# Performance work log

Hardware: AMD Instinct MI355X
Metric: run time of the kernel (lower is better)

Reference implementation:

```python
import jax, jax.numpy as jnp
import numpy as np
from jax import lax

N = 2048
BS = 64
NUM_ITR = 25


def setup_inputs() -> dict:
    key = jax.random.key(0)
    k1, k2, k3, k4, k5 = jax.random.split(key, 5)
    scale = 0.5 / np.sqrt(N)  # keep iteration matrices contractive so the recurrence stays bounded
    H = jax.random.normal(k1, (N, N), dtype=jnp.float32) / np.sqrt(N)
    Dinv = jax.random.normal(k2, (N, N), dtype=jnp.float32) * scale
    U = jax.random.normal(k3, (N, N), dtype=jnp.float32) * scale
    invM = jax.random.normal(k4, (N, N), dtype=jnp.float32) * scale
    y = jax.random.normal(k5, (BS, N), dtype=jnp.float32)
    return {"num_itr": NUM_ITR, "bs": BS, "y": y, "H": H, "Dinv": Dinv, "U": U, "invM": invM}


def reference(num_itr, bs, y, H, Dinv, U, invM):
    n = H.shape[0]
    s0 = jnp.zeros((bs, n), dtype=y.dtype)
    yMF = y @ H.T                 # [bs, n]
    s_init = yMF @ Dinv           # initial Gauss-Seidel estimate

    def step(s, _):
        s_next = (yMF - s @ U) @ invM
        return s_next, s_next

    s_final, traj_iters = lax.scan(step, s_init, None, length=num_itr)
    # traj matches the torch list: [zeros, s_1, ..., s_num_itr]
    traj = jnp.concatenate([s0[None], traj_iters], axis=0)  # [num_itr+1, bs, n]
    return s_final, traj
```

## Files before the change

kernel.cpp:

```cpp
#include <hip/hip_runtime.h>
#include <hip/hip_bf16.h>

#define NDIM 2048
#define BS   64
#define NM4  (NDIM * NDIM / 4)
#define BSN  ((size_t)BS * NDIM)
#define SMEM_BYTES 69632

typedef __bf16 bf16_t;
typedef __bf16 bf16x4 __attribute__((ext_vector_type(4)));
typedef __bf16 bf16x8 __attribute__((ext_vector_type(8)));
typedef float  f32x4  __attribute__((ext_vector_type(4)));

__device__ __forceinline__ void gload16(const void* g, void* lds) {
  __builtin_amdgcn_global_load_lds(
      (const __attribute__((address_space(1))) void*)g,
      (__attribute__((address_space(3))) void*)lds, 16, 0, 0);
}

#define WB4 asm volatile("s_waitcnt vmcnt(4)\n\ts_barrier" ::: "memory")
#define WB2 asm volatile("s_waitcnt vmcnt(2)\n\ts_barrier" ::: "memory")
#define WB0 asm volatile("s_waitcnt vmcnt(0)\n\ts_barrier" ::: "memory")

__global__ __launch_bounds__(512) void prep(
    const float* __restrict__ H, const float* __restrict__ U,
    const float* __restrict__ Dinv, const float* __restrict__ invM,
    const float* __restrict__ y,
    bf16_t* __restrict__ H16, bf16_t* __restrict__ U16,
    bf16_t* __restrict__ Dt, bf16_t* __restrict__ iMt,
    bf16_t* __restrict__ y16, float* __restrict__ traj0) {
  __shared__ bf16_t tile[64][72];
  int b = blockIdx.x, tid = threadIdx.x;
  if (b < 1024) {
#pragma unroll
    for (int i = 0; i < 4; ++i) {
      int idx = b * 2048 + i * 512 + tid;
      const float* src = (idx < NM4) ? H : U;
      bf16_t* dst = (idx < NM4) ? H16 : U16;
      int j = (idx < NM4) ? idx : idx - NM4;
      float4 v = ((const float4*)src)[j];
      bf16x4 o = {(bf16_t)v.x, (bf16_t)v.y, (bf16_t)v.z, (bf16_t)v.w};
      ((bf16x4*)dst)[j] = o;
    }
    int yi = b * 512 + tid;
    if (yi < BS * NDIM / 4) {
      float4 w = ((const float4*)y)[yi];
      bf16x4 o2 = {(bf16_t)w.x, (bf16_t)w.y, (bf16_t)w.z, (bf16_t)w.w};
      ((bf16x4*)y16)[yi] = o2;
      ((float4*)traj0)[yi] = make_float4(0.f, 0.f, 0.f, 0.f);
    }
  } else {
    int id = b - 1024;
    const float* src = (id < 1024) ? Dinv : invM;
    bf16_t* dst = (id < 1024) ? Dt : iMt;
    id &= 1023;
    int bx = id & 31, by = id >> 5;
    int r = tid >> 3, c8 = (tid & 7) * 8;
    const float* sp = src + (size_t)(by * 64 + r) * NDIM + bx * 64 + c8;
    float4 v0 = *(const float4*)sp;
    float4 v1 = *(const float4*)(sp + 4);
    bf16_t* t = &tile[r][c8];
    t[0] = (bf16_t)v0.x; t[1] = (bf16_t)v0.y; t[2] = (bf16_t)v0.z; t[3] = (bf16_t)v0.w;
    t[4] = (bf16_t)v1.x; t[5] = (bf16_t)v1.y; t[6] = (bf16_t)v1.z; t[7] = (bf16_t)v1.w;
    __syncthreads();
    bf16x8 o;
#pragma unroll
    for (int j = 0; j < 8; ++j) o[j] = tile[c8 + j][r];
    *(bf16x8*)(dst + (size_t)(bx * 64 + r) * NDIM + by * 64 + c8) = o;
  }
}

__device__ __forceinline__ void wgemm_role(
    const bf16_t* __restrict__ A, const bf16_t* __restrict__ Bt,
    bf16_t* __restrict__ C, int blk, char* smem) {
  int tid = threadIdx.x, lane = tid & 63, wave = tid >> 6;
  int m0 = (blk >> 4) * 128, n0 = (blk & 15) * 128;
  int rl = lane & 15, q = lane >> 4;
  const bf16_t* Ag = A  + (size_t)(m0 + wave * 16 + rl) * NDIM + q * 8;
  const bf16_t* Bg = Bt + (size_t)(n0 + wave * 16 + rl) * NDIM + q * 8;
  char* ldsA = smem + wave * 1024;
  char* ldsB = smem + 8192 + wave * 1024;

  f32x4 acc[2][4];
#pragma unroll
  for (int i = 0; i < 2; ++i)
#pragma unroll
    for (int j = 0; j < 4; ++j) acc[i][j] = (f32x4){0.f, 0.f, 0.f, 0.f};

  int wr2 = (wave & 3) * 2, wc4 = (wave >> 2) * 4;

#define STAGE(s)                                  \
  {                                               \
    int _b = (s) & 3, _k = (s) * 32;              \
    gload16(Ag + _k, ldsA + _b * 16384);          \
    gload16(Bg + _k, ldsB + _b * 16384);          \
  }
#define COMPUTE(bb)                                                            \
  {                                                                            \
    bf16x8* As = (bf16x8*)(smem + (bb) * 16384);                               \
    bf16x8* Bs = (bf16x8*)(smem + (bb) * 16384 + 8192);                        \
    bf16x8 af0 = As[wr2 * 64 + lane];                                          \
    bf16x8 af1 = As[(wr2 + 1) * 64 + lane];                                    \
    bf16x8 bf0 = Bs[wc4 * 64 + lane];                                          \
    bf16x8 bf1 = Bs[(wc4 + 1) * 64 + lane];                                    \
    bf16x8 bf2 = Bs[(wc4 + 2) * 64 + lane];                                    \
    bf16x8 bf3 = Bs[(wc4 + 3) * 64 + lane];                                    \
    acc[0][0] = __builtin_amdgcn_mfma_f32_16x16x32_bf16(af0, bf0, acc[0][0], 0, 0, 0); \
    acc[0][1] = __builtin_amdgcn_mfma_f32_16x16x32_bf16(af0, bf1, acc[0][1], 0, 0, 0); \
    acc[0][2] = __builtin_amdgcn_mfma_f32_16x16x32_bf16(af0, bf2, acc[0][2], 0, 0, 0); \
    acc[0][3] = __builtin_amdgcn_mfma_f32_16x16x32_bf16(af0, bf3, acc[0][3], 0, 0, 0); \
    acc[1][0] = __builtin_amdgcn_mfma_f32_16x16x32_bf16(af1, bf0, acc[1][0], 0, 0, 0); \
    acc[1][1] = __builtin_amdgcn_mfma_f32_16x16x32_bf16(af1, bf1, acc[1][1], 0, 0, 0); \
    acc[1][2] = __builtin_amdgcn_mfma_f32_16x16x32_bf16(af1, bf2, acc[1][2], 0, 0, 0); \
    acc[1][3] = __builtin_amdgcn_mfma_f32_16x16x32_bf16(af1, bf3, acc[1][3], 0, 0, 0); \
  }

  STAGE(0); STAGE(1); STAGE(2);
  int s = 3;
#pragma unroll 1
  for (int k = 0; k < 60; k += 4) {
    WB4; STAGE(s); ++s; COMPUTE(0);
    WB4; STAGE(s); ++s; COMPUTE(1);
    WB4; STAGE(s); ++s; COMPUTE(2);
    WB4; STAGE(s); ++s; COMPUTE(3);
  }
  WB4; STAGE(63); COMPUTE(0);
  WB4; COMPUTE(1);
  WB2; COMPUTE(2);
  WB0; COMPUTE(3);
#undef STAGE
#undef COMPUTE

#pragma unroll
  for (int i = 0; i < 2; ++i)
#pragma unroll
    for (int j = 0; j < 4; ++j)
#pragma unroll
      for (int r = 0; r < 4; ++r)
        C[(size_t)(m0 + (wr2 + i) * 16 + q * 4 + r) * NDIM + n0 + (wc4 + j) * 16 + rl] =
            (bf16_t)acc[i][j][r];
}

__device__ __forceinline__ void skinny_role(
    const bf16_t* __restrict__ A, const bf16_t* __restrict__ Bt, int n0, char* smem,
    const float* __restrict__ add, float sign,
    float* o32, float* o32b, bf16_t* o16) {
  int tid = threadIdx.x, lane = tid & 63, wave = tid >> 6;
  int rl = lane & 15, q = lane >> 4;
#pragma unroll
  for (int i = 0; i < 8; ++i) {
    const bf16_t* g = Bt + (size_t)(n0 + rl) * NDIM + (i * 8 + wave) * 32 + q * 8;
    gload16(g, smem + (size_t)(i * 512 + wave * 64) * 16);
  }
  __syncthreads();

  int ms = (wave & 3) * 16, kh = wave >> 2;
  const bf16x8* Ap = (const bf16x8*)(A + (size_t)(ms + rl) * NDIM) + q + kh * 128;
  const bf16x8* Bp = (const bf16x8*)smem + lane + kh * 2048;

  f32x4 acc[8];
#pragma unroll
  for (int i = 0; i < 8; ++i) acc[i] = (f32x4){0.f, 0.f, 0.f, 0.f};
#pragma unroll
  for (int c = 0; c < 32; ++c)
    acc[c & 7] = __builtin_amdgcn_mfma_f32_16x16x32_bf16(Ap[c * 4], Bp[c * 64], acc[c & 7], 0, 0, 0);
  f32x4 s = ((acc[0] + acc[1]) + (acc[2] + acc[3])) + ((acc[4] + acc[5]) + (acc[6] + acc[7]));

  f32x4* red = (f32x4*)(smem + 65536);
  if (wave >= 4) red[(wave & 3) * 64 + lane] = s;
  __syncthreads();
  if (wave < 4) {
    s += red[wave * 64 + lane];
    int mrow = ms + q * 4, col = n0 + rl;
#pragma unroll
    for (int r = 0; r < 4; ++r) {
      size_t o = (size_t)(mrow + r) * NDIM + col;
      float v = sign * s[r];
      if (add) v += add[o];
      if (o32)  o32[o]  = v;
      if (o32b) o32b[o] = v;
      if (o16)  o16[o]  = (bf16_t)v;
    }
  }
}

__device__ __forceinline__ void transpose_role(const bf16_t* __restrict__ src,
                                               bf16_t* __restrict__ dst, int blk, char* smem) {
  bf16_t (*tile)[72] = (bf16_t(*)[72])smem;
  int tid = threadIdx.x;
  int bx = blk & 31, by = blk >> 5;
  int r = tid >> 3, c8 = (tid & 7) * 8;
  *(bf16x8*)&tile[r][c8] = *(const bf16x8*)(src + (size_t)(by * 64 + r) * NDIM + bx * 64 + c8);
  __syncthreads();
  bf16x8 o;
#pragma unroll
  for (int j = 0; j < 8; ++j) o[j] = tile[c8 + j][r];
  *(bf16x8*)(dst + (size_t)(bx * 64 + r) * NDIM + by * 64 + c8) = o;
}

__global__ __launch_bounds__(512, 4) void megaA(
    const bf16_t* __restrict__ U16, const bf16_t* __restrict__ iMt16,
    const bf16_t* __restrict__ y16, const bf16_t* __restrict__ H16,
    bf16_t* __restrict__ Wrm, bf16_t* __restrict__ yMF16) {
  __shared__ char smem[SMEM_BYTES];
  int b = blockIdx.x;
  if (b < 256) wgemm_role(U16, iMt16, Wrm, b, smem);
  else         skinny_role(y16, H16, (b - 256) * 16, smem, nullptr, 1.f, nullptr, nullptr, yMF16);
}

__global__ __launch_bounds__(512, 4) void megaB(
    const bf16_t* __restrict__ Wrm, const bf16_t* __restrict__ yMF16,
    const bf16_t* __restrict__ iMt16, const bf16_t* __restrict__ Dt16,
    bf16_t* __restrict__ Wt, float* __restrict__ c32, bf16_t* __restrict__ c16,
    bf16_t* __restrict__ z0) {
  __shared__ char smem[SMEM_BYTES];
  int b = blockIdx.x;
  if (b < 1024)      transpose_role(Wrm, Wt, b, smem);
  else if (b < 1152) skinny_role(yMF16, iMt16, (b - 1024) * 16, smem, nullptr, 1.f, c32, nullptr, c16);
  else               skinny_role(yMF16, Dt16, (b - 1152) * 16, smem, nullptr, 1.f, nullptr, nullptr, z0);
}

__global__ __launch_bounds__(512, 4) void megaC(
    const bf16_t* __restrict__ Wt, const bf16_t* __restrict__ Wrm,
    const bf16_t* __restrict__ z0, const bf16_t* __restrict__ c16,
    const float* __restrict__ c32,
    bf16_t* __restrict__ W2t, float* __restrict__ traj1, bf16_t* __restrict__ z0b,
    float* __restrict__ c2_32, bf16_t* __restrict__ c2_16) {
  __shared__ char smem[SMEM_BYTES];
  int b = blockIdx.x;
  if (b < 256)      wgemm_role(Wt, Wrm, W2t, b, smem);
  else if (b < 384) skinny_role(z0, Wt, (b - 256) * 16, smem, c32, -1.f, traj1, nullptr, z0b);
  else              skinny_role(c16, Wt, (b - 384) * 16, smem, c32, -1.f, c2_32, nullptr, c2_16);
}

__global__ __launch_bounds__(512, 4) void megaD(
    const bf16_t* __restrict__ W2t, const bf16_t* __restrict__ z0,
    const bf16_t* __restrict__ c2_16, const float* __restrict__ c2_32,
    bf16_t* __restrict__ W2rm, float* __restrict__ traj2, float* __restrict__ traj3,
    bf16_t* __restrict__ zA, float* __restrict__ c4_32) {
  __shared__ char smem[SMEM_BYTES];
  int b = blockIdx.x;
  if (b < 1024)      transpose_role(W2t, W2rm, b, smem);
  else if (b < 1152) skinny_role(z0, W2t, (b - 1024) * 16, smem, c2_32, 1.f, traj2, nullptr, zA);
  else if (b < 1280) skinny_role(z0 + BSN, W2t, (b - 1152) * 16, smem, c2_32, 1.f, traj3, nullptr, zA + BSN);
  else               skinny_role(c2_16, W2t, (b - 1280) * 16, smem, c2_32, 1.f, c4_32, nullptr, nullptr);
}

__global__ __launch_bounds__(512, 4) void megaE(
    const bf16_t* __restrict__ W2t, const bf16_t* __restrict__ W2rm,
    const bf16_t* __restrict__ zA_in, const float* __restrict__ c2_32,
    bf16_t* __restrict__ W4t, float* __restrict__ traj4, float* __restrict__ traj5,
    bf16_t* __restrict__ zA) {
  __shared__ char smem[SMEM_BYTES];
  int b = blockIdx.x;
  if (b < 256)      wgemm_role(W2t, W2rm, W4t, b, smem);
  else if (b < 384) skinny_role(zA_in, W2t, (b - 256) * 16, smem, c2_32, 1.f, traj4, nullptr, zA + 2 * BSN);
  else              skinny_role(zA_in + BSN, W2t, (b - 384) * 16, smem, c2_32, 1.f, traj5, nullptr, zA + 3 * BSN);
}

__global__ __launch_bounds__(512, 4) void quad_step(
    const bf16_t* __restrict__ zin, const bf16_t* __restrict__ W4t,
    const float* __restrict__ c4_32, float* __restrict__ trajb,
    bf16_t* __restrict__ zout, float* __restrict__ sfin) {
  __shared__ char smem[SMEM_BYTES];
  int b = blockIdx.x, ci = b & 3, p = b >> 2;
  skinny_role(zin + (size_t)ci * BSN, W4t, p * 16, smem, c4_32, 1.f,
              trajb + (size_t)ci * BSN, (ci == 3) ? sfin : nullptr,
              zout + (size_t)ci * BSN);
}

extern "C" void kernel_launch(void* const* d_in, const int* in_sizes, int n_in,
                              void* d_out, int out_size, void* d_ws, size_t ws_size,
                              hipStream_t stream) {
  const float* y    = (const float*)d_in[2];
  const float* H    = (const float*)d_in[3];
  const float* Dinv = (const float*)d_in[4];
  const float* U    = (const float*)d_in[5];
  const float* invM = (const float*)d_in[6];

  float* out     = (float*)d_out;
  float* s_final = out;
  float* traj    = out + BSN;

  char* ws = (char*)d_ws;
  size_t off = 0;
  auto alloc = [&](size_t bytes) -> void* {
    void* p = ws + off;
    off += (bytes + 255) & ~(size_t)255;
    return p;
  };
  bf16_t* U16   = (bf16_t*)alloc((size_t)NDIM * NDIM * 2);
  bf16_t* Dt16  = (bf16_t*)alloc((size_t)NDIM * NDIM * 2);
  bf16_t* iMt16 = (bf16_t*)alloc((size_t)NDIM * NDIM * 2);
  bf16_t* H16   = (bf16_t*)alloc((size_t)NDIM * NDIM * 2);
  bf16_t* Wrm   = (bf16_t*)alloc((size_t)NDIM * NDIM * 2);
  bf16_t* Wt    = (bf16_t*)alloc((size_t)NDIM * NDIM * 2);
  bf16_t* y16   = (bf16_t*)alloc(BSN * 2);
  bf16_t* yMF16 = (bf16_t*)alloc(BSN * 2);
  bf16_t* c16   = (bf16_t*)alloc(BSN * 2);
  bf16_t* c2_16 = (bf16_t*)alloc(BSN * 2);
  float*  c32   = (float*)alloc(BSN * 4);
  float*  c2_32 = (float*)alloc(BSN * 4);
  float*  c4_32 = (float*)alloc(BSN * 4);
  bf16_t* z0    = (bf16_t*)alloc(2 * BSN * 2);
  bf16_t* zA    = (bf16_t*)alloc(4 * BSN * 2);
  bf16_t* zB    = (bf16_t*)alloc(4 * BSN * 2);
  bf16_t* W2t   = H16;
  bf16_t* W2rm  = U16;
  bf16_t* W4t   = Dt16;

  prep<<<3072, 512, 0, stream>>>(H, U, Dinv, invM, y, H16, U16, Dt16, iMt16, y16, traj);
  megaA<<<384, 512, 0, stream>>>(U16, iMt16, y16, H16, Wrm, yMF16);
  megaB<<<1280, 512, 0, stream>>>(Wrm, yMF16, iMt16, Dt16, Wt, c32, c16, z0);
  megaC<<<512, 512, 0, stream>>>(Wt, Wrm, z0, c16, c32, W2t, traj + BSN, z0 + BSN, c2_32, c2_16);
  megaD<<<1408, 512, 0, stream>>>(W2t, z0, c2_16, c2_32, W2rm, traj + 2 * BSN, traj + 3 * BSN,
                                  zA, c4_32);
  megaE<<<512, 512, 0, stream>>>(W2t, W2rm, zA, c2_32, W4t, traj + 4 * BSN, traj + 5 * BSN, zA);

  bf16_t* zcur = zA;
  bf16_t* znxt = zB;
  for (int g = 0; g < 5; ++g) {
    float* sfin = (g == 4) ? s_final : nullptr;
    quad_step<<<512, 512, 0, stream>>>(zcur, W4t, c4_32, traj + (size_t)(6 + 4 * g) * BSN,
                                       znxt, sfin);
    bf16_t* tmp = zcur; zcur = znxt; znxt = tmp;
  }
}
```

Baseline: 389.2 us.

## Fuse transposes into GEMM epilogue and use inline-asm LDS reads

The dense GEMM role now writes a transposed copy of its output tile through an LDS staging buffer, so the separate transpose blocks in megaB and megaD are removed and those launches shrink to only the skinny products. The GEMM inner loop also switches to inline-asm ds_read_b128 with immediate offsets and an explicit lgkmcnt wait. This drops two full-matrix read/write passes but adds an extra epilogue with barriers and a second global store per GEMM block. The explicit waitcnt may also limit how well the compiler overlaps LDS reads with MFMAs.

```diff
diff --git a/kernel.cpp b/kernel.cpp
--- a/kernel.cpp
+++ b/kernel.cpp
@@ -16,6 +16,9 @@
   __builtin_amdgcn_global_load_lds(
       (const __attribute__((address_space(1))) void*)g,
       (__attribute__((address_space(3))) void*)lds, 16, 0, 0);
+}
+__device__ __forceinline__ uint32_t lds_off(void* p) {
+  return (uint32_t)(uintptr_t)(__attribute__((address_space(3))) void*)p;
 }
 
 #define WB4 asm volatile("s_waitcnt vmcnt(4)\n\ts_barrier" ::: "memory")
@@ -72,7 +75,7 @@
 
 __device__ __forceinline__ void wgemm_role(
     const bf16_t* __restrict__ A, const bf16_t* __restrict__ Bt,
-    bf16_t* __restrict__ C, int blk, char* smem) {
+    bf16_t* __restrict__ C, bf16_t* __restrict__ Ct, int blk, char* smem) {
   int tid = threadIdx.x, lane = tid & 63, wave = tid >> 6;
   int m0 = (blk >> 4) * 128, n0 = (blk & 15) * 128;
   int rl = lane & 15, q = lane >> 4;
@@ -81,13 +84,15 @@
   char* ldsA = smem + wave * 1024;
   char* ldsB = smem + 8192 + wave * 1024;
 
+  int wr2 = (wave & 3) * 2, wc4 = (wave >> 2) * 4;
+  uint32_t abase = lds_off(smem) + wr2 * 1024 + lane * 16;
+  uint32_t bbase = lds_off(smem) + 8192 + wc4 * 1024 + lane * 16;
+
   f32x4 acc[2][4];
 #pragma unroll
   for (int i = 0; i < 2; ++i)
 #pragma unroll
     for (int j = 0; j < 4; ++j) acc[i][j] = (f32x4){0.f, 0.f, 0.f, 0.f};
-
-  int wr2 = (wave & 3) * 2, wc4 = (wave >> 2) * 4;
 
 #define STAGE(s)                                  \
   {                                               \
@@ -97,22 +102,26 @@
   }
 #define COMPUTE(bb)                                                            \
   {                                                                            \
-    bf16x8* As = (bf16x8*)(smem + (bb) * 16384);                               \
-    bf16x8* Bs = (bf16x8*)(smem + (bb) * 16384 + 8192);                        \
-    bf16x8 af0 = As[wr2 * 64 + lane];                                          \
-    bf16x8 af1 = As[(wr2 + 1) * 64 + lane];                                    \
-    bf16x8 bf0 = Bs[wc4 * 64 + lane];                                          \
-    bf16x8 bf1 = Bs[(wc4 + 1) * 64 + lane];                                    \
-    bf16x8 bf2 = Bs[(wc4 + 2) * 64 + lane];                                    \
-    bf16x8 bf3 = Bs[(wc4 + 3) * 64 + lane];                                    \
-    acc[0][0] = __builtin_amdgcn_mfma_f32_16x16x32_bf16(af0, bf0, acc[0][0], 0, 0, 0); \
-    acc[0][1] = __builtin_amdgcn_mfma_f32_16x16x32_bf16(af0, bf1, acc[0][1], 0, 0, 0); \
-    acc[0][2] = __builtin_amdgcn_mfma_f32_16x16x32_bf16(af0, bf2, acc[0][2], 0, 0, 0); \
-    acc[0][3] = __builtin_amdgcn_mfma_f32_16x16x32_bf16(af0, bf3, acc[0][3], 0, 0, 0); \
-    acc[1][0] = __builtin_amdgcn_mfma_f32_16x16x32_bf16(af1, bf0, acc[1][0], 0, 0, 0); \
-    acc[1][1] = __builtin_amdgcn_mfma_f32_16x16x32_bf16(af1, bf1, acc[1][1], 0, 0, 0); \
-    acc[1][2] = __builtin_amdgcn_mfma_f32_16x16x32_bf16(af1, bf2, acc[1][2], 0, 0, 0); \
-    acc[1][3] = __builtin_amdgcn_mfma_f32_16x16x32_bf16(af1, bf3, acc[1][3], 0, 0, 0); \
+    uint32_t av = abase + (bb) * 16384;                                        \
+    uint32_t bv = bbase + (bb) * 16384;                                        \
+    bf16x8 af0, af1, bg0, bg1, bg2, bg3;                                       \
+    asm volatile("ds_read_b128 %0, %1"             : "=v"(af0) : "v"(av));     \
+    asm volatile("ds_read_b128 %0, %1 offset:1024" : "=v"(af1) : "v"(av));     \
+    asm volatile("ds_read_b128 %0, %1"             : "=v"(bg0) : "v"(bv));     \
+    asm volatile("ds_read_b128 %0, %1 offset:1024" : "=v"(bg1) : "v"(bv));     \
+    asm volatile("ds_read_b128 %0, %1 offset:2048" : "=v"(bg2) : "v"(bv));     \
+    asm volatile("ds_read_b128 %0, %1 offset:3072" : "=v"(bg3) : "v"(bv));     \
+    asm volatile("s_waitcnt lgkmcnt(0)"                                        \
+                 : "+v"(af0), "+v"(af1), "+v"(bg0), "+v"(bg1), "+v"(bg2),      \
+                   "+v"(bg3));                                                 \
+    acc[0][0] = __builtin_amdgcn_mfma_f32_16x16x32_bf16(af0, bg0, acc[0][0], 0, 0, 0); \
+    acc[0][1] = __builtin_amdgcn_mfma_f32_16x16x32_bf16(af0, bg1, acc[0][1], 0, 0, 0); \
+    acc[0][2] = __builtin_amdgcn_mfma_f32_16x16x32_bf16(af0, bg2, acc[0][2], 0, 0, 0); \
+    acc[0][3] = __builtin_amdgcn_mfma_f32_16x16x32_bf16(af0, bg3, acc[0][3], 0, 0, 0); \
+    acc[1][0] = __builtin_amdgcn_mfma_f32_16x16x32_bf16(af1, bg0, acc[1][0], 0, 0, 0); \
+    acc[1][1] = __builtin_amdgcn_mfma_f32_16x16x32_bf16(af1, bg1, acc[1][1], 0, 0, 0); \
+    acc[1][2] = __builtin_amdgcn_mfma_f32_16x16x32_bf16(af1, bg2, acc[1][2], 0, 0, 0); \
+    acc[1][3] = __builtin_amdgcn_mfma_f32_16x16x32_bf16(af1, bg3, acc[1][3], 0, 0, 0); \
   }
 
   STAGE(0); STAGE(1); STAGE(2);
@@ -139,6 +148,24 @@
       for (int r = 0; r < 4; ++r)
         C[(size_t)(m0 + (wr2 + i) * 16 + q * 4 + r) * NDIM + n0 + (wc4 + j) * 16 + rl] =
             (bf16_t)acc[i][j][r];
+
+  if (Ct) {
+    __syncthreads();
+    bf16_t (*tileT)[136] = (bf16_t(*)[136])smem;
+#pragma unroll
+    for (int i = 0; i < 2; ++i)
+#pragma unroll
+      for (int j = 0; j < 4; ++j)
+#pragma unroll
+        for (int r = 0; r < 4; ++r)
+          tileT[(wc4 + j) * 16 + rl][(wr2 + i) * 16 + q * 4 + r] = (bf16_t)acc[i][j][r];
+    __syncthreads();
+#pragma unroll
+    for (int t = 0; t < 4; ++t) {
+      int v = t * 512 + tid, row = v >> 4, c8 = (v & 15) * 8;
+      *(bf16x8*)(Ct + (size_t)(n0 + row) * NDIM + m0 + c8) = *(bf16x8*)&tileT[row][c8];
+    }
+  }
 }
 
 __device__ __forceinline__ void skinny_role(
@@ -184,51 +211,36 @@
   }
 }
 
-__device__ __forceinline__ void transpose_role(const bf16_t* __restrict__ src,
-                                               bf16_t* __restrict__ dst, int blk, char* smem) {
-  bf16_t (*tile)[72] = (bf16_t(*)[72])smem;
-  int tid = threadIdx.x;
-  int bx = blk & 31, by = blk >> 5;
-  int r = tid >> 3, c8 = (tid & 7) * 8;
-  *(bf16x8*)&tile[r][c8] = *(const bf16x8*)(src + (size_t)(by * 64 + r) * NDIM + bx * 64 + c8);
-  __syncthreads();
-  bf16x8 o;
-#pragma unroll
-  for (int j = 0; j < 8; ++j) o[j] = tile[c8 + j][r];
-  *(bf16x8*)(dst + (size_t)(bx * 64 + r) * NDIM + by * 64 + c8) = o;
-}
-
 __global__ __launch_bounds__(512, 4) void megaA(
     const bf16_t* __restrict__ U16, const bf16_t* __restrict__ iMt16,
     const bf16_t* __restrict__ y16, const bf16_t* __restrict__ H16,
-    bf16_t* __restrict__ Wrm, bf16_t* __restrict__ yMF16) {
-  __shared__ char smem[SMEM_BYTES];
-  int b = blockIdx.x;
-  if (b < 256) wgemm_role(U16, iMt16, Wrm, b, smem);
+    bf16_t* __restrict__ Wrm, bf16_t* __restrict__ Wt, bf16_t* __restrict__ yMF16) {
+  __shared__ char smem[SMEM_BYTES];
+  int b = blockIdx.x;
+  if (b < 256) wgemm_role(U16, iMt16, Wrm, Wt, b, smem);
   else         skinny_role(y16, H16, (b - 256) * 16, smem, nullptr, 1.f, nullptr, nullptr, yMF16);
 }
 
 __global__ __launch_bounds__(512, 4) void megaB(
-    const bf16_t* __restrict__ Wrm, const bf16_t* __restrict__ yMF16,
-    const bf16_t* __restrict__ iMt16, const bf16_t* __restrict__ Dt16,
-    bf16_t* __restrict__ Wt, float* __restrict__ c32, bf16_t* __restrict__ c16,
-    bf16_t* __restrict__ z0) {
-  __shared__ char smem[SMEM_BYTES];
-  int b = blockIdx.x;
-  if (b < 1024)      transpose_role(Wrm, Wt, b, smem);
-  else if (b < 1152) skinny_role(yMF16, iMt16, (b - 1024) * 16, smem, nullptr, 1.f, c32, nullptr, c16);
-  else               skinny_role(yMF16, Dt16, (b - 1152) * 16, smem, nullptr, 1.f, nullptr, nullptr, z0);
+    const bf16_t* __restrict__ yMF16, const bf16_t* __restrict__ iMt16,
+    const bf16_t* __restrict__ Dt16,
+    float* __restrict__ c32, bf16_t* __restrict__ c16, bf16_t* __restrict__ z0) {
+  __shared__ char smem[SMEM_BYTES];
+  int b = blockIdx.x;
+  if (b < 128) skinny_role(yMF16, iMt16, b * 16, smem, nullptr, 1.f, c32, nullptr, c16);
+  else         skinny_role(yMF16, Dt16, (b - 128) * 16, smem, nullptr, 1.f, nullptr, nullptr, z0);
 }
 
 __global__ __launch_bounds__(512, 4) void megaC(
     const bf16_t* __restrict__ Wt, const bf16_t* __restrict__ Wrm,
     const bf16_t* __restrict__ z0, const bf16_t* __restrict__ c16,
     const float* __restrict__ c32,
-    bf16_t* __restrict__ W2t, float* __restrict__ traj1, bf16_t* __restrict__ z0b,
+    bf16_t* __restrict__ W2t, bf16_t* __restrict__ W2rm,
+    float* __restrict__ traj1, bf16_t* __restrict__ z0b,
     float* __restrict__ c2_32, bf16_t* __restrict__ c2_16) {
   __shared__ char smem[SMEM_BYTES];
   int b = blockIdx.x;
-  if (b < 256)      wgemm_role(Wt, Wrm, W2t, b, smem);
+  if (b < 256)      wgemm_role(Wt, Wrm, W2t, W2rm, b, smem);
   else if (b < 384) skinny_role(z0, Wt, (b - 256) * 16, smem, c32, -1.f, traj1, nullptr, z0b);
   else              skinny_role(c16, Wt, (b - 384) * 16, smem, c32, -1.f, c2_32, nullptr, c2_16);
 }
@@ -236,14 +248,13 @@
 __global__ __launch_bounds__(512, 4) void megaD(
     const bf16_t* __restrict__ W2t, const bf16_t* __restrict__ z0,
     const bf16_t* __restrict__ c2_16, const float* __restrict__ c2_32,
-    bf16_t* __restrict__ W2rm, float* __restrict__ traj2, float* __restrict__ traj3,
+    float* __restrict__ traj2, float* __restrict__ traj3,
     bf16_t* __restrict__ zA, float* __restrict__ c4_32) {
   __shared__ char smem[SMEM_BYTES];
   int b = blockIdx.x;
-  if (b < 1024)      transpose_role(W2t, W2rm, b, smem);
-  else if (b < 1152) skinny_role(z0, W2t, (b - 1024) * 16, smem, c2_32, 1.f, traj2, nullptr, zA);
-  else if (b < 1280) skinny_role(z0 + BSN, W2t, (b - 1152) * 16, smem, c2_32, 1.f, traj3, nullptr, zA + BSN);
-  else               skinny_role(c2_16, W2t, (b - 1280) * 16, smem, c2_32, 1.f, c4_32, nullptr, nullptr);
+  if (b < 128)      skinny_role(z0, W2t, b * 16, smem, c2_32, 1.f, traj2, nullptr, zA);
+  else if (b < 256) skinny_role(z0 + BSN, W2t, (b - 128) * 16, smem, c2_32, 1.f, traj3, nullptr, zA + BSN);
+  else              skinny_role(c2_16, W2t, (b - 256) * 16, smem, c2_32, 1.f, c4_32, nullptr, nullptr);
 }
 
 __global__ __launch_bounds__(512, 4) void megaE(
@@ -253,7 +264,7 @@
     bf16_t* __restrict__ zA) {
   __shared__ char smem[SMEM_BYTES];
   int b = blockIdx.x;
-  if (b < 256)      wgemm_role(W2t, W2rm, W4t, b, smem);
+  if (b < 256)      wgemm_role(W2t, W2rm, W4t, nullptr, b, smem);
   else if (b < 384) skinny_role(zA_in, W2t, (b - 256) * 16, smem, c2_32, 1.f, traj4, nullptr, zA + 2 * BSN);
   else              skinny_role(zA_in + BSN, W2t, (b - 384) * 16, smem, c2_32, 1.f, traj5, nullptr, zA + 3 * BSN);
 }
@@ -310,11 +321,12 @@
   bf16_t* W4t   = Dt16;
 
   prep<<<3072, 512, 0, stream>>>(H, U, Dinv, invM, y, H16, U16, Dt16, iMt16, y16, traj);
-  megaA<<<384, 512, 0, stream>>>(U16, iMt16, y16, H16, Wrm, yMF16);
-  megaB<<<1280, 512, 0, stream>>>(Wrm, yMF16, iMt16, Dt16, Wt, c32, c16, z0);
-  megaC<<<512, 512, 0, stream>>>(Wt, Wrm, z0, c16, c32, W2t, traj + BSN, z0 + BSN, c2_32, c2_16);
-  megaD<<<1408, 512, 0, stream>>>(W2t, z0, c2_16, c2_32, W2rm, traj + 2 * BSN, traj + 3 * BSN,
-                                  zA, c4_32);
+  megaA<<<384, 512, 0, stream>>>(U16, iMt16, y16, H16, Wrm, Wt, yMF16);
+  megaB<<<256, 512, 0, stream>>>(yMF16, iMt16, Dt16, c32, c16, z0);
+  megaC<<<512, 512, 0, stream>>>(Wt, Wrm, z0, c16, c32, W2t, W2rm,
+                                 traj + BSN, z0 + BSN, c2_32, c2_16);
+  megaD<<<384, 512, 0, stream>>>(W2t, z0, c2_16, c2_32, traj + 2 * BSN, traj + 3 * BSN,
+                                 zA, c4_32);
   megaE<<<512, 512, 0, stream>>>(W2t, W2rm, zA, c2_32, W4t, traj + 4 * BSN, traj + 5 * BSN, zA);
 
   bf16_t* zcur = zA;
```

After: 385.2 us. About the same (-1.0%).
